# Optimization experiments

Measured on AMD Instinct MI355X. Metric: run time of the kernel, lower is better.

## Reference

```python
import jax, jax.numpy as jnp
import numpy as np

CAP = 15.0
EPS = 1e-6

def _soft_cap(x):
    return CAP * jnp.tanh(x / CAP)

def _rms_norm(x, w):
    xf = x.astype(jnp.float32)
    var = jnp.mean(xf * xf, axis=-1, keepdims=True)
    return w * (xf * jax.lax.rsqrt(var + EPS)).astype(x.dtype)

def setup_inputs() -> dict:
    key = jax.random.key(0)
    ks = jax.random.split(key, 6)
    B, S, D, P = 4, 2048, 2048, int(2048 * 1.333)
    sd = 1.0 / np.sqrt(D)
    sp = 1.0 / np.sqrt(P)
    return {
        "x": jax.random.normal(ks[0], (B, S, D), dtype=jnp.float32),
        "hidden_state": jnp.zeros((B, P), dtype=jnp.float32),
        "Wi": jax.random.normal(ks[1], (P, D), dtype=jnp.float32) * sd,
        "Wf": jax.random.normal(ks[2], (P, D), dtype=jnp.float32) * sd,
        "Wo": jax.random.normal(ks[3], (P, D), dtype=jnp.float32) * sd,
        "Wc": jax.random.normal(ks[4], (P, D), dtype=jnp.float32) * sd,
        "Wout": jax.random.normal(ks[5], (D, P), dtype=jnp.float32) * sp,
        "ln_weight": jnp.ones((D,), dtype=jnp.float32),
    }

def reference(x, hidden_state, Wi, Wf, Wo, Wc, Wout, ln_weight):
    residual = x
    xn = _rms_norm(x, ln_weight)                       # (B,S,D)
    i_gate = jax.nn.sigmoid(_soft_cap(jnp.einsum('bsd,pd->bsp', xn, Wi)))
    f_gate = jax.nn.sigmoid(_soft_cap(jnp.einsum('bsd,pd->bsp', xn, Wf)))
    o_gate = jax.nn.sigmoid(_soft_cap(jnp.einsum('bsd,pd->bsp', xn, Wo)))
    c_input = jnp.einsum('bsd,pd->bsp', xn, Wc)

    def step(h, gates):
        i_t, f_t, o_t, c_t = gates
        h = f_t * h + i_t * jnp.tanh(c_t)
        return h, o_t * jnp.tanh(h)

    # scan over time axis: move seq to leading dim
    seq = (jnp.swapaxes(i_gate, 0, 1), jnp.swapaxes(f_gate, 0, 1),
           jnp.swapaxes(o_gate, 0, 1), jnp.swapaxes(c_input, 0, 1))
    h_final, outs = jax.lax.scan(step, hidden_state, seq)
    output = jnp.swapaxes(outs, 0, 1)                  # (B,S,P)
    out = residual + jnp.einsum('bsp,dp->bsd', output, Wout)
    return out, h_final
```

## Files before the change

kernel.cpp:

```cpp
#include <hip/hip_runtime.h>
#include <hip/hip_bf16.h>
#include <stdint.h>
#include <stdio.h>

#define B_ 4
#define S_ 2048
#define D_ 2048
#define P_ 2729
#define NP 2816
#define M_ (B_ * S_)

#define SCHUNK 128
#define NCHUNK (S_ / SCHUNK)

#define SX_Q   28.0f
#define SW_Q   1152.0f
#define SO_Q   127.0f
#define SW2_Q  1327.0f
#define INV_GATE (1.0f / (SX_Q * SW_Q))
#define INV_OUT  (1.0f / (SO_Q * SW2_Q))

typedef __attribute__((ext_vector_type(4))) int iv4;

static __device__ __forceinline__ float bf2f(unsigned short u) {
  union { unsigned int i; float f; } c;
  c.i = ((unsigned int)u) << 16;
  return c.f;
}
static __device__ __forceinline__ unsigned short f2bf(float f) {
  union { __hip_bfloat16 h; unsigned short u; } c;
  c.h = __float2bfloat16(f);
  return c.u;
}
static __device__ __forceinline__ float fast_tanh(float x) {
  return 1.0f - 2.0f / (__expf(2.0f * x) + 1.0f);
}
static __device__ __forceinline__ float gate_act(float z) {
  float sc = 15.0f * fast_tanh(z * (1.0f / 15.0f));
  return 1.0f / (1.0f + __expf(-sc));
}
static __device__ __forceinline__ int quant8(float v, float s) {
  int q = __float2int_rn(v * s);
  q = max(-127, min(127, q));
  return q & 255;
}

static __device__ __forceinline__ void gload_lds16(const void* g, void* l) {
  __builtin_amdgcn_global_load_lds(
      (const __attribute__((address_space(1))) unsigned int*)g,
      (__attribute__((address_space(3))) unsigned int*)l, 16, 0, 0);
}

__global__ __launch_bounds__(256) void rmsnorm_kernel(const float* __restrict__ x,
                                                      const float* __restrict__ w,
                                                      signed char* __restrict__ xq) {
  int row = blockIdx.x;
  const float4* xr = (const float4*)(x + (size_t)row * D_);
  int t = threadIdx.x;
  float4 v0 = xr[t];
  float4 v1 = xr[t + 256];
  float ss = v0.x * v0.x + v0.y * v0.y + v0.z * v0.z + v0.w * v0.w +
             v1.x * v1.x + v1.y * v1.y + v1.z * v1.z + v1.w * v1.w;
#pragma unroll
  for (int off = 32; off > 0; off >>= 1) ss += __shfl_down(ss, off);
  __shared__ float red[4];
  if ((t & 63) == 0) red[t >> 6] = ss;
  __syncthreads();
  float scale = rsqrtf((red[0] + red[1] + red[2] + red[3]) * (1.0f / (float)D_) + 1e-6f);
  const float4* wp = (const float4*)w;
  float4 w0 = wp[t], w1 = wp[t + 256];
  int p0 = quant8(v0.x * scale * w0.x, SX_Q) | (quant8(v0.y * scale * w0.y, SX_Q) << 8) |
           (quant8(v0.z * scale * w0.z, SX_Q) << 16) | (quant8(v0.w * scale * w0.w, SX_Q) << 24);
  int p1 = quant8(v1.x * scale * w1.x, SX_Q) | (quant8(v1.y * scale * w1.y, SX_Q) << 8) |
           (quant8(v1.z * scale * w1.z, SX_Q) << 16) | (quant8(v1.w * scale * w1.w, SX_Q) << 24);
  int* xo = (int*)(xq + (size_t)row * D_);
  xo[t] = p0;
  xo[t + 256] = p1;
}

__global__ __launch_bounds__(256) void convert_gate_w(const float* __restrict__ Wi,
                                                      const float* __restrict__ Wf,
                                                      const float* __restrict__ Wo,
                                                      const float* __restrict__ Wc,
                                                      signed char* __restrict__ Wq) {
  int g = blockIdx.z;
  const float* W = (g == 0) ? Wi : (g == 1) ? Wf : (g == 2) ? Wo : Wc;
  size_t u = (size_t)blockIdx.x * 256 + threadIdx.x;
  int j = (int)(u >> 9);
  int q = (int)(u & 511);
  int packed = 0;
  if (j < P_) {
    float4 v = ((const float4*)(W + (size_t)j * D_))[q];
    packed = quant8(v.x, SW_Q) | (quant8(v.y, SW_Q) << 8) |
             (quant8(v.z, SW_Q) << 16) | (quant8(v.w, SW_Q) << 24);
  }
  int* dst = (int*)(Wq + (size_t)g * NP * D_ + (size_t)j * D_) + q;
  *dst = packed;
}

__global__ __launch_bounds__(256) void convert_wout(const float* __restrict__ Wout,
                                                    signed char* __restrict__ Wq) {
  size_t u = (size_t)blockIdx.x * 256 + threadIdx.x;
  if (u >= (size_t)D_ * NP) return;
  int d = (int)(u / NP);
  int p = (int)(u - (size_t)d * NP);
  int q = 0;
  if (p < P_) q = quant8(Wout[(size_t)d * P_ + p], SW2_Q);
  Wq[u] = (signed char)q;
}

template <int LD, int KTOT>
static __device__ __forceinline__ void gemm_core_i8(const signed char* __restrict__ A,
                                                    const signed char* __restrict__ Bm,
                                                    int tile_m, int tile_n,
                                                    unsigned char* lds,
                                                    iv4 (&acc)[8][4]) {
  const int t = threadIdx.x;
  const int lane = t & 63;
  const int w = t >> 6;
  const int wr = w >> 2, wc = w & 3;
  const int frow = lane & 15;
  const int g = lane >> 4;

  unsigned char* buf0 = lds;
  unsigned char* buf1 = lds + 65536;

  const signed char* gsrc[8];
  int loff[8];
#pragma unroll
  for (int q = 0; q < 8; ++q) {
    int u = q * 512 + t;
    int isB = u >> 11;
    int uu = u & 2047;
    int row = uu >> 3;
    int phys = uu & 7;
    int s = phys ^ (row & 7);
    gsrc[q] = (isB ? (Bm + (size_t)(tile_n + row) * LD)
                   : (A + (size_t)(tile_m + row) * LD)) + s * 16;
    loff[q] = isB * 32768 + uu * 16;
  }

  auto STAGE = [&](int k0, unsigned char* dst) {
#pragma unroll
    for (int q = 0; q < 8; ++q) gload_lds16(gsrc[q] + k0, dst + loff[q]);
  };

  const int px0 = ((g ^ (frow & 7)) << 4);
  const int px1 = (((4 | g) ^ (frow & 7)) << 4);
  const int aBase = (wr * 128 + frow) << 7;
  const int bBase = 32768 + ((wc * 64 + frow) << 7);

  auto COMPUTE = [&](const unsigned char* buf) {
#pragma unroll
    for (int kk = 0; kk < 2; ++kk) {
      const int px = kk ? px1 : px0;
      iv4 bf[4];
#pragma unroll
      for (int nf = 0; nf < 4; ++nf)
        bf[nf] = *(const iv4*)(buf + bBase + (nf << 11) + px);
      iv4 af[8];
#pragma unroll
      for (int mf = 0; mf < 8; ++mf)
        af[mf] = *(const iv4*)(buf + aBase + (mf << 11) + px);
#pragma unroll
      for (int mf = 0; mf < 8; ++mf)
#pragma unroll
        for (int nf = 0; nf < 4; ++nf)
          acc[mf][nf] = __builtin_amdgcn_mfma_i32_16x16x64_i8(af[mf], bf[nf], acc[mf][nf], 0, 0, 0);
    }
  };

  STAGE(0, buf0);
  __syncthreads();
  for (int k0 = 0; k0 < KTOT; k0 += 256) {
    const bool haveC = (k0 + 256 < KTOT);
    STAGE(k0 + 128, buf1);
    COMPUTE(buf0);
    __syncthreads();
    if (haveC) STAGE(k0 + 256, buf0);
    COMPUTE(buf1);
    if (haveC) __syncthreads();
  }
}

__global__ __launch_bounds__(512, 1) void gemm_gates(const signed char* __restrict__ A,
                                                     const signed char* __restrict__ Wq,
                                                     __hip_bfloat16* __restrict__ G) {
  __shared__ unsigned char lds[131072];
  int gate = blockIdx.z;
  int lin = blockIdx.x + 11 * blockIdx.y;
  int xcd = lin & 7;
  int idx = lin >> 3;
  int bx = idx % 11;
  int by = xcd * 4 + idx / 11;
  int tile_n = bx * 256;
  int tile_m = by * 256;

  const signed char* Bm = Wq + (size_t)gate * NP * D_;
  __hip_bfloat16* Gg = G + (size_t)gate * M_ * NP;

  iv4 acc[8][4];
#pragma unroll
  for (int i = 0; i < 8; ++i)
#pragma unroll
    for (int j = 0; j < 4; ++j) acc[i][j] = (iv4){0, 0, 0, 0};

  gemm_core_i8<D_, D_>(A, Bm, tile_m, tile_n, lds, acc);

  int lane = threadIdx.x & 63;
  int w = threadIdx.x >> 6;
  int wr = w >> 2, wc = w & 3;
  int g = lane >> 4;
#pragma unroll
  for (int mf = 0; mf < 8; ++mf) {
    int mbase = tile_m + wr * 128 + mf * 16 + (g << 2);
#pragma unroll
    for (int nf = 0; nf < 4; ++nf) {
      int n = tile_n + wc * 64 + nf * 16 + (lane & 15);
      bool valid = (n < P_);
#pragma unroll
      for (int r = 0; r < 4; ++r) {
        float z = (float)acc[mf][nf][r] * INV_GATE;
        float val = (gate == 3) ? fast_tanh(z) : gate_act(z);
        if (!valid) val = 0.0f;
        Gg[(size_t)(mbase + r) * NP + n] = __float2bfloat16(val);
      }
    }
  }
}

__global__ __launch_bounds__(512, 1) void gemm_out(const signed char* __restrict__ A,
                                                   const signed char* __restrict__ Bw,
                                                   const float* __restrict__ X,
                                                   float* __restrict__ Out) {
  __shared__ unsigned char lds[131072];
  int lin = blockIdx.x + 8 * blockIdx.y;
  int xcd = lin & 7;
  int idx = lin >> 3;
  int bx = idx & 7;
  int by = xcd * 4 + (idx >> 3);
  int tile_n = bx * 256;
  int tile_m = by * 256;

  iv4 acc[8][4];
#pragma unroll
  for (int i = 0; i < 8; ++i)
#pragma unroll
    for (int j = 0; j < 4; ++j) acc[i][j] = (iv4){0, 0, 0, 0};

  gemm_core_i8<NP, NP>(A, Bw, tile_m, tile_n, lds, acc);

  int lane = threadIdx.x & 63;
  int w = threadIdx.x >> 6;
  int wr = w >> 2, wc = w & 3;
  int g = lane >> 4;
#pragma unroll
  for (int mf = 0; mf < 8; ++mf) {
    int mbase = tile_m + wr * 128 + mf * 16 + (g << 2);
#pragma unroll
    for (int nf = 0; nf < 4; ++nf) {
      int n = tile_n + wc * 64 + nf * 16 + (lane & 15);
#pragma unroll
      for (int r = 0; r < 4; ++r) {
        size_t o = (size_t)(mbase + r) * D_ + n;
        Out[o] = X[o] + (float)acc[mf][nf][r] * INV_OUT;
      }
    }
  }
}

__global__ __launch_bounds__(256) void scan_pass1(const __hip_bfloat16* __restrict__ G,
                                                  float* __restrict__ Aa, float* __restrict__ Bb) {
  int idx = blockIdx.x * 256 + threadIdx.x;
  int c = blockIdx.y;
  int b = idx / NP, p = idx - b * NP;
  size_t base = ((size_t)(b * S_ + c * SCHUNK)) * NP + p;
  const unsigned short* gi = (const unsigned short*)G + base;
  const size_t gs = (size_t)M_ * NP;
  const unsigned short* gf = gi + gs;
  const unsigned short* gc = gi + 3 * gs;
  float a = 1.f, acc = 0.f;
#pragma unroll 8
  for (int s = 0; s < SCHUNK; ++s) {
    size_t off = (size_t)s * NP;
    float fv = bf2f(gf[off]);
    float u = bf2f(gi[off]) * bf2f(gc[off]);
    acc = fv * acc + u;
    a *= fv;
  }
  int o = c * (B_ * NP) + idx;
  Aa[o] = a;
  Bb[o] = acc;
}

__global__ __launch_bounds__(256) void scan_mid(const float* __restrict__ Aa,
                                                const float* __restrict__ Bb,
                                                const float* __restrict__ h0,
                                                float* __restrict__ Hs,
                                                float* __restrict__ hfin) {
  int idx = blockIdx.x * 256 + threadIdx.x;
  int b = idx / NP, p = idx - b * NP;
  float h = (p < P_) ? h0[b * P_ + p] : 0.f;
#pragma unroll
  for (int c = 0; c < NCHUNK; ++c) {
    int o = c * (B_ * NP) + idx;
    Hs[o] = h;
    h = Aa[o] * h + Bb[o];
  }
  if (p < P_) hfin[b * P_ + p] = h;
}

__global__ __launch_bounds__(256) void scan_pass2(const __hip_bfloat16* __restrict__ G,
                                                  const float* __restrict__ Hs,
                                                  signed char* __restrict__ outq) {
  int idx = blockIdx.x * 256 + threadIdx.x;
  int c = blockIdx.y;
  int b = idx / NP, p = idx - b * NP;
  size_t base = ((size_t)(b * S_ + c * SCHUNK)) * NP + p;
  const unsigned short* gi = (const unsigned short*)G + base;
  const size_t gs = (size_t)M_ * NP;
  const unsigned short* gf = gi + gs;
  const unsigned short* go = gi + 2 * gs;
  const unsigned short* gc = gi + 3 * gs;
  signed char* ob = outq + base;
  float h = Hs[c * (B_ * NP) + idx];
#pragma unroll 4
  for (int s = 0; s < SCHUNK; ++s) {
    size_t off = (size_t)s * NP;
    float u = bf2f(gi[off]) * bf2f(gc[off]);
    h = bf2f(gf[off]) * h + u;
    float v = bf2f(go[off]) * fast_tanh(h);
    int q = __float2int_rn(v * SO_Q);
    q = max(-127, min(127, q));
    ob[off] = (signed char)q;
  }
}

extern "C" void kernel_launch(void* const* d_in, const int* in_sizes, int n_in,
                              void* d_out, int out_size, void* d_ws, size_t ws_size,
                              hipStream_t stream) {
  const float* x    = (const float*)d_in[0];
  const float* h0   = (const float*)d_in[1];
  const float* Wi   = (const float*)d_in[2];
  const float* Wf   = (const float*)d_in[3];
  const float* Wo   = (const float*)d_in[4];
  const float* Wc   = (const float*)d_in[5];
  const float* Wout = (const float*)d_in[6];
  const float* lnw  = (const float*)d_in[7];
  float* out  = (float*)d_out;
  float* hfin = out + (size_t)M_ * D_;

  const size_t xn_off    = 0;
  const size_t wq_off    = (size_t)M_ * D_;
  const size_t gates_off = wq_off + (size_t)4 * NP * D_;
  const size_t need = gates_off + (size_t)4 * M_ * NP * 2;
  if (ws_size < need) {
    fprintf(stderr, "kernel_launch: ws too small (%zu < %zu)\n", ws_size, need);
    return;
  }
  char* ws = (char*)d_ws;
  signed char* xn_q   = (signed char*)(ws + xn_off);
  signed char* Wq     = (signed char*)(ws + wq_off);
  __hip_bfloat16* Gg  = (__hip_bfloat16*)(ws + gates_off);
  signed char* outq   = (signed char*)ws;
  signed char* Woutq  = (signed char*)(ws + (size_t)M_ * NP);
  float* scr = (float*)(ws + (size_t)M_ * NP + (size_t)D_ * NP);
  float* Aa = scr;
  float* Bb = Aa + NCHUNK * B_ * NP;
  float* Hs = Bb + NCHUNK * B_ * NP;

  convert_gate_w<<<dim3(NP * 512 / 256, 1, 4), 256, 0, stream>>>(Wi, Wf, Wo, Wc, Wq);
  rmsnorm_kernel<<<M_, 256, 0, stream>>>(x, lnw, xn_q);
  gemm_gates<<<dim3(NP / 256, M_ / 256, 4), 512, 0, stream>>>(xn_q, Wq, Gg);
  convert_wout<<<(int)(((size_t)D_ * NP + 255) / 256), 256, 0, stream>>>(Wout, Woutq);
  scan_pass1<<<dim3(B_ * NP / 256, NCHUNK), 256, 0, stream>>>(Gg, Aa, Bb);
  scan_mid<<<B_ * NP / 256, 256, 0, stream>>>(Aa, Bb, h0, Hs, hfin);
  scan_pass2<<<dim3(B_ * NP / 256, NCHUNK), 256, 0, stream>>>(Gg, Hs, outq);
  gemm_out<<<dim3(D_ / 256, M_ / 256), 512, 0, stream>>>(outq, Woutq, x, out);
}
```

Before: 434.7 us.

## Store gate activations as int8 and vectorize scan passes over four channels

The gates GEMM epilogue now quantizes its activations to int8 with a fixed scale of 127 instead of writing bf16. The scan passes read packed 4-byte words, so each thread handles four channels with int loads and packed int stores. This halves the gate tensor traffic written by the GEMM and read twice by the scans, and cuts the scan grid by four. In exchange, the gates carry coarser quantization error (about 1/254 absolute), which compounds through the forget-gate product over long chunks.

```diff
diff --git a/kernel.cpp b/kernel.cpp
--- a/kernel.cpp
+++ b/kernel.cpp
@@ -15,23 +15,15 @@
 
 #define SX_Q   28.0f
 #define SW_Q   1152.0f
+#define SG_Q   127.0f
 #define SO_Q   127.0f
 #define SW2_Q  1327.0f
 #define INV_GATE (1.0f / (SX_Q * SW_Q))
 #define INV_OUT  (1.0f / (SO_Q * SW2_Q))
+#define IGQ      (1.0f / SG_Q)
 
 typedef __attribute__((ext_vector_type(4))) int iv4;
 
-static __device__ __forceinline__ float bf2f(unsigned short u) {
-  union { unsigned int i; float f; } c;
-  c.i = ((unsigned int)u) << 16;
-  return c.f;
-}
-static __device__ __forceinline__ unsigned short f2bf(float f) {
-  union { __hip_bfloat16 h; unsigned short u; } c;
-  c.h = __float2bfloat16(f);
-  return c.u;
-}
 static __device__ __forceinline__ float fast_tanh(float x) {
   return 1.0f - 2.0f / (__expf(2.0f * x) + 1.0f);
 }
@@ -185,7 +177,7 @@
 
 __global__ __launch_bounds__(512, 1) void gemm_gates(const signed char* __restrict__ A,
                                                      const signed char* __restrict__ Wq,
-                                                     __hip_bfloat16* __restrict__ G) {
+                                                     signed char* __restrict__ G) {
   __shared__ unsigned char lds[131072];
   int gate = blockIdx.z;
   int lin = blockIdx.x + 11 * blockIdx.y;
@@ -197,7 +189,7 @@
   int tile_m = by * 256;
 
   const signed char* Bm = Wq + (size_t)gate * NP * D_;
-  __hip_bfloat16* Gg = G + (size_t)gate * M_ * NP;
+  signed char* Gq = G + (size_t)gate * M_ * NP;
 
   iv4 acc[8][4];
 #pragma unroll
@@ -223,7 +215,9 @@
         float z = (float)acc[mf][nf][r] * INV_GATE;
         float val = (gate == 3) ? fast_tanh(z) : gate_act(z);
         if (!valid) val = 0.0f;
-        Gg[(size_t)(mbase + r) * NP + n] = __float2bfloat16(val);
+        int q = __float2int_rn(val * SG_Q);
+        q = max(-127, min(127, q));
+        Gq[(size_t)(mbase + r) * NP + n] = (signed char)q;
       }
     }
   }
@@ -269,28 +263,37 @@
   }
 }
 
-__global__ __launch_bounds__(256) void scan_pass1(const __hip_bfloat16* __restrict__ G,
+__global__ __launch_bounds__(256) void scan_pass1(const signed char* __restrict__ G,
                                                   float* __restrict__ Aa, float* __restrict__ Bb) {
-  int idx = blockIdx.x * 256 + threadIdx.x;
+  int idx4 = blockIdx.x * 256 + threadIdx.x;
   int c = blockIdx.y;
-  int b = idx / NP, p = idx - b * NP;
-  size_t base = ((size_t)(b * S_ + c * SCHUNK)) * NP + p;
-  const unsigned short* gi = (const unsigned short*)G + base;
+  int b = idx4 / (NP / 4);
+  int p4 = (idx4 - b * (NP / 4)) * 4;
+  size_t base = ((size_t)(b * S_ + c * SCHUNK)) * NP + p4;
+  const signed char* gi = G + base;
   const size_t gs = (size_t)M_ * NP;
-  const unsigned short* gf = gi + gs;
-  const unsigned short* gc = gi + 3 * gs;
-  float a = 1.f, acc = 0.f;
-#pragma unroll 8
+  const signed char* gf = gi + gs;
+  const signed char* gc = gi + 3 * gs;
+  float a[4] = {1.f, 1.f, 1.f, 1.f};
+  float acc[4] = {0.f, 0.f, 0.f, 0.f};
+#pragma unroll 4
   for (int s = 0; s < SCHUNK; ++s) {
     size_t off = (size_t)s * NP;
-    float fv = bf2f(gf[off]);
-    float u = bf2f(gi[off]) * bf2f(gc[off]);
-    acc = fv * acc + u;
-    a *= fv;
-  }
-  int o = c * (B_ * NP) + idx;
-  Aa[o] = a;
-  Bb[o] = acc;
+    int qi = *(const int*)(gi + off);
+    int qf = *(const int*)(gf + off);
+    int qc = *(const int*)(gc + off);
+#pragma unroll
+    for (int j = 0; j < 4; ++j) {
+      float fv = (float)((signed char)(qf >> (8 * j))) * IGQ;
+      float iv = (float)((signed char)(qi >> (8 * j))) * IGQ;
+      float cv = (float)((signed char)(qc >> (8 * j))) * IGQ;
+      acc[j] = fv * acc[j] + iv * cv;
+      a[j] *= fv;
+    }
+  }
+  int o = c * (B_ * NP) + b * NP + p4;
+  *(float4*)(Aa + o) = make_float4(a[0], a[1], a[2], a[3]);
+  *(float4*)(Bb + o) = make_float4(acc[0], acc[1], acc[2], acc[3]);
 }
 
 __global__ __launch_bounds__(256) void scan_mid(const float* __restrict__ Aa,
@@ -310,29 +313,43 @@
   if (p < P_) hfin[b * P_ + p] = h;
 }
 
-__global__ __launch_bounds__(256) void scan_pass2(const __hip_bfloat16* __restrict__ G,
+__global__ __launch_bounds__(256) void scan_pass2(const signed char* __restrict__ G,
                                                   const float* __restrict__ Hs,
                                                   signed char* __restrict__ outq) {
-  int idx = blockIdx.x * 256 + threadIdx.x;
+  int idx4 = blockIdx.x * 256 + threadIdx.x;
   int c = blockIdx.y;
-  int b = idx / NP, p = idx - b * NP;
-  size_t base = ((size_t)(b * S_ + c * SCHUNK)) * NP + p;
-  const unsigned short* gi = (const unsigned short*)G + base;
+  int b = idx4 / (NP / 4);
+  int p4 = (idx4 - b * (NP / 4)) * 4;
+  size_t base = ((size_t)(b * S_ + c * SCHUNK)) * NP + p4;
+  const signed char* gi = G + base;
   const size_t gs = (size_t)M_ * NP;
-  const unsigned short* gf = gi + gs;
-  const unsigned short* go = gi + 2 * gs;
-  const unsigned short* gc = gi + 3 * gs;
+  const signed char* gf = gi + gs;
+  const signed char* go = gi + 2 * gs;
+  const signed char* gc = gi + 3 * gs;
   signed char* ob = outq + base;
-  float h = Hs[c * (B_ * NP) + idx];
-#pragma unroll 4
+  float4 hs = *(const float4*)(Hs + c * (B_ * NP) + b * NP + p4);
+  float h[4] = {hs.x, hs.y, hs.z, hs.w};
+#pragma unroll 2
   for (int s = 0; s < SCHUNK; ++s) {
     size_t off = (size_t)s * NP;
-    float u = bf2f(gi[off]) * bf2f(gc[off]);
-    h = bf2f(gf[off]) * h + u;
-    float v = bf2f(go[off]) * fast_tanh(h);
-    int q = __float2int_rn(v * SO_Q);
-    q = max(-127, min(127, q));
-    ob[off] = (signed char)q;
+    int qi = *(const int*)(gi + off);
+    int qf = *(const int*)(gf + off);
+    int qo = *(const int*)(go + off);
+    int qc = *(const int*)(gc + off);
+    int packed = 0;
+#pragma unroll
+    for (int j = 0; j < 4; ++j) {
+      float fv = (float)((signed char)(qf >> (8 * j))) * IGQ;
+      float iv = (float)((signed char)(qi >> (8 * j))) * IGQ;
+      float cv = (float)((signed char)(qc >> (8 * j))) * IGQ;
+      float ov = (float)((signed char)(qo >> (8 * j))) * IGQ;
+      h[j] = fv * h[j] + iv * cv;
+      float v = ov * fast_tanh(h[j]);
+      int q = __float2int_rn(v * SO_Q);
+      q = max(-127, min(127, q));
+      packed |= (q & 255) << (8 * j);
+    }
+    *(int*)(ob + off) = packed;
   }
 }
 
@@ -353,7 +370,7 @@
   const size_t xn_off    = 0;
   const size_t wq_off    = (size_t)M_ * D_;
   const size_t gates_off = wq_off + (size_t)4 * NP * D_;
-  const size_t need = gates_off + (size_t)4 * M_ * NP * 2;
+  const size_t need = gates_off + (size_t)4 * M_ * NP;
   if (ws_size < need) {
     fprintf(stderr, "kernel_launch: ws too small (%zu < %zu)\n", ws_size, need);
     return;
@@ -361,7 +378,7 @@
   char* ws = (char*)d_ws;
   signed char* xn_q   = (signed char*)(ws + xn_off);
   signed char* Wq     = (signed char*)(ws + wq_off);
-  __hip_bfloat16* Gg  = (__hip_bfloat16*)(ws + gates_off);
+  signed char* Gq     = (signed char*)(ws + gates_off);
   signed char* outq   = (signed char*)ws;
   signed char* Woutq  = (signed char*)(ws + (size_t)M_ * NP);
   float* scr = (float*)(ws + (size_t)M_ * NP + (size_t)D_ * NP);
@@ -371,10 +388,10 @@
 
   convert_gate_w<<<dim3(NP * 512 / 256, 1, 4), 256, 0, stream>>>(Wi, Wf, Wo, Wc, Wq);
   rmsnorm_kernel<<<M_, 256, 0, stream>>>(x, lnw, xn_q);
-  gemm_gates<<<dim3(NP / 256, M_ / 256, 4), 512, 0, stream>>>(xn_q, Wq, Gg);
+  gemm_gates<<<dim3(NP / 256, M_ / 256, 4), 512, 0, stream>>>(xn_q, Wq, Gq);
   convert_wout<<<(int)(((size_t)D_ * NP + 255) / 256), 256, 0, stream>>>(Wout, Woutq);
-  scan_pass1<<<dim3(B_ * NP / 256, NCHUNK), 256, 0, stream>>>(Gg, Aa, Bb);
+  scan_pass1<<<dim3(B_ * NP / 4 / 256, NCHUNK), 256, 0, stream>>>(Gq, Aa, Bb);
   scan_mid<<<B_ * NP / 256, 256, 0, stream>>>(Aa, Bb, h0, Hs, hfin);
-  scan_pass2<<<dim3(B_ * NP / 256, NCHUNK), 256, 0, stream>>>(Gg, Hs, outq);
+  scan_pass2<<<dim3(B_ * NP / 4 / 256, NCHUNK), 256, 0, stream>>>(Gq, Hs, outq);
   gemm_out<<<dim3(D_ / 256, M_ / 256), 512, 0, stream>>>(outq, Woutq, x, out);
 }
```

Result: slower. 458.6 us (+5.5%).
